# Performance work log

Measured on AMD Instinct MI355X. Metric: run time of the kernel, lower is better.

Reference implementation:

```python
import jax, jax.numpy as jnp
import numpy as np
from jax import lax

MAX_W = 4           # max_subword_block_width
DOWNSAMPLE = 2      # downsample_rate


def setup_inputs() -> dict:
    key = jax.random.key(0)
    k1, k2, k3, k4 = jax.random.split(key, 4)
    B, E, L, K = 8, 512, 4096, 5
    x = jax.random.normal(k1, (B, E, L), dtype=jnp.float32)
    conv_w = jax.random.normal(k2, (E, E, K), dtype=jnp.float32) * (1.0 / np.sqrt(E * K))
    conv_b = jax.random.normal(k3, (E,), dtype=jnp.float32) * 0.02
    score_w = jax.random.normal(k4, (E,), dtype=jnp.float32) * (1.0 / np.sqrt(E))
    return {"x": x, "conv_w": conv_w, "conv_b": conv_b, "score_w": score_w}


def reference(x, conv_w, conv_b, score_w):
    B, E, L = x.shape  # `length` captured BEFORE conv, as in the torch code
    # pre-GBST conv, VALID padding: length becomes L - K + 1
    y = lax.conv_general_dilated(
        x, conv_w, window_strides=(1,), padding='VALID',
        dimension_numbers=('NCH', 'OIH', 'NCH')) + conv_b[None, :, None]
    L2 = y.shape[-1]
    seqs, scores = [], []
    for w in range(1, MAX_W + 1):
        pad = (-L2) % w
        yp = jnp.pad(y, ((0, 0), (0, 0), (0, pad)))  # zero-pad to multiple of w
        nb = yp.shape[-1] // w
        pooled = yp.reshape(B, E, nb, w).mean(-1)          # avg_pool1d(kernel=w, stride=w)
        sc = jnp.einsum('ben,e->bn', pooled, score_w)      # Linear(E,1,bias=False)
        rs = jnp.repeat(pooled, w, axis=-1)                # repeat_interleave
        rsc = jnp.repeat(sc, w, axis=-1)
        cur = rs.shape[-1]
        if cur < L:  # re-pad with zeros up to the ORIGINAL (pre-conv) length
            rs = jnp.pad(rs, ((0, 0), (0, 0), (0, L - cur)))
            rsc = jnp.pad(rsc, ((0, 0), (0, L - cur)))
        seqs.append(rs[:, :, :L])
        scores.append(rsc[:, :L])
    S = jnp.stack(seqs, axis=-1)                           # [B,E,L,W]
    A = jax.nn.softmax(jnp.stack(scores, axis=-1), axis=-1)  # [B,L,W]
    out = jnp.einsum('belw,blw->bel', S, A)                # softmax-weighted combine
    r = DOWNSAMPLE
    Ld = (L // r) * r
    out = out[:, :, :Ld].reshape(B, E, L // r, r).mean(-1)  # final avg_pool1d
    return out
```

## Files before the change

### kernel.cpp

```cpp
#include <hip/hip_runtime.h>
#include <stdint.h>

#define E_DIM 512
#define L_IN  4096
#define L_OUT 4092
#define KW    5
#define B_DIM 8
#define L2P   4096
#define L_DS  2048
#define LP    4160

typedef __attribute__((ext_vector_type(8))) short short8;
typedef __attribute__((ext_vector_type(4))) float f32x4;

__device__ __forceinline__ unsigned short f2bf(float f) {
    uint32_t u = __float_as_uint(f);
    u += 0x7fffu + ((u >> 16) & 1);
    return (unsigned short)(u >> 16);
}
__device__ __forceinline__ float bf2f(unsigned short h) {
    return __uint_as_float((uint32_t)h << 16);
}

__global__ __launch_bounds__(256)
void xt_kernel(const float* __restrict__ x, unsigned short* __restrict__ Xt)
{
    const int b  = blockIdx.z;
    const int i0 = blockIdx.y * 64;
    const int l0 = blockIdx.x * 64;
    __shared__ float T[64][65];
    const int tid = threadIdx.x;

    const int ir = tid >> 4;
    const int cq = (tid & 15) * 4;
    #pragma unroll
    for (int jj = 0; jj < 4; ++jj) {
        int i = jj * 16 + ir;
        float4 v = make_float4(0.f, 0.f, 0.f, 0.f);
        if (l0 < L_IN)
            v = *reinterpret_cast<const float4*>(
                &x[((size_t)b * E_DIM + i0 + i) * L_IN + l0 + cq]);
        T[i][cq + 0] = v.x; T[i][cq + 1] = v.y;
        T[i][cq + 2] = v.z; T[i][cq + 3] = v.w;
    }
    __syncthreads();
    const int h  = tid & 31;
    const int rq = tid >> 5;
    #pragma unroll
    for (int j = 0; j < 8; ++j) {
        int lr = j * 8 + rq;
        ushort2 o;
        o.x = f2bf(T[2 * h][lr]);
        o.y = f2bf(T[2 * h + 1][lr]);
        *reinterpret_cast<ushort2*>(
            &Xt[((size_t)b * LP + l0 + lr) * E_DIM + i0 + 2 * h]) = o;
    }
}

__global__ __launch_bounds__(256)
void wt_kernel(const float* __restrict__ w, unsigned short* __restrict__ Wt)
{
    int idx = blockIdx.x * 256 + threadIdx.x;
    if (idx >= E_DIM * E_DIM) return;
    #pragma unroll
    for (int k = 0; k < KW; ++k)
        Wt[(size_t)k * E_DIM * E_DIM + idx] = f2bf(w[(size_t)idx * KW + k]);
}

#define XS_BYTES (144 * 64)
#define WS_OFF   XS_BYTES
#define WS_BYTES (5 * 128 * 64)
#define LDS_BYTES (XS_BYTES + WS_BYTES)
#define N_XCH (XS_BYTES / 1024)
#define N_CH  (LDS_BYTES / 1024)

__global__ __launch_bounds__(256, 3)
void conv_mfma(const unsigned short* __restrict__ Xt,
               const unsigned short* __restrict__ Wt,
               const float* __restrict__ bias,
               const float* __restrict__ sw,
               unsigned short* __restrict__ y,
               float* __restrict__ sp)
{
    __shared__ __align__(16) unsigned char lds[LDS_BYTES];
    const int l0 = blockIdx.x * 128;
    const int e0 = blockIdx.y * 128;
    const int b  = blockIdx.z;
    const int tid  = threadIdx.x;
    const int lane = tid & 63;
    const int wv   = tid >> 6;
    const int wr = wv >> 1, wc = wv & 1;
    const int lr = lane & 15, lg = lane >> 4;
    const int ln4r = lane >> 2;
    const int ln4c = (lane & 3) * 8;

    f32x4 acc[4][4] = {};

    for (int ks = 0; ks < 16; ++ks) {
        const int i0 = ks * 32;
        __syncthreads();
        for (int cch = wv; cch < N_CH; cch += 4) {
            void* lp = (void*)(lds + cch * 1024);
            const unsigned short* gp;
            if (cch < N_XCH) {
                int row = cch * 16 + ln4r;
                gp = Xt + ((size_t)b * LP + l0 + row) * E_DIM + i0 + ln4c;
            } else {
                int rk = (cch - N_XCH) * 16 + ln4r;
                int k = rk >> 7, er = rk & 127;
                gp = Wt + ((size_t)k * E_DIM + e0 + er) * E_DIM + i0 + ln4c;
            }
            __builtin_amdgcn_global_load_lds(
                (const __attribute__((address_space(1))) void*)gp,
                (__attribute__((address_space(3))) void*)lp,
                16, 0, 0);
        }
        __syncthreads();
        #pragma unroll
        for (int kt = 0; kt < KW; ++kt) {
            short8 aF[4], bF[4];
            #pragma unroll
            for (int m = 0; m < 4; ++m)
                aF[m] = *reinterpret_cast<const short8*>(
                    &lds[WS_OFF + (kt * 128 + wr * 64 + m * 16 + lr) * 64 + lg * 16]);
            #pragma unroll
            for (int n = 0; n < 4; ++n)
                bF[n] = *reinterpret_cast<const short8*>(
                    &lds[(wc * 64 + n * 16 + lr + kt) * 64 + lg * 16]);
            #pragma unroll
            for (int m = 0; m < 4; ++m)
                #pragma unroll
                for (int n = 0; n < 4; ++n)
                    acc[m][n] = __builtin_amdgcn_mfma_f32_16x16x32_bf16(
                        aF[m], bF[n], acc[m][n], 0, 0, 0);
        }
    }

    float spn[4] = {0.f, 0.f, 0.f, 0.f};
    #pragma unroll
    for (int m = 0; m < 4; ++m)
        #pragma unroll
        for (int q = 0; q < 4; ++q) {
            int e = e0 + wr * 64 + m * 16 + lg * 4 + q;
            float bv = bias[e];
            float wv_s = sw[e];
            unsigned short* yr =
                y + ((size_t)b * E_DIM + e) * L2P + l0 + wc * 64 + lr;
            #pragma unroll
            for (int n = 0; n < 4; ++n) {
                float v = acc[m][n][q] + bv;
                yr[n * 16] = f2bf(v);
                spn[n] = fmaf(v, wv_s, spn[n]);
            }
        }
    #pragma unroll
    for (int n = 0; n < 4; ++n) {
        float p = spn[n];
        p += __shfl_xor(p, 16);
        p += __shfl_xor(p, 32);
        if (lane < 16) {
            int l = l0 + wc * 64 + n * 16 + lane;
            sp[((size_t)b * L2P + l) * 8 + blockIdx.y * 2 + wr] = p;
        }
    }
}

__global__ __launch_bounds__(256)
void weight_kernel(const float* __restrict__ sp, float* __restrict__ A)
{
    const int b  = blockIdx.y;
    const int l0 = blockIdx.x * 256;
    const int tid = threadIdx.x;
    __shared__ float sl[260];

    for (int idx = tid; idx < 260; idx += 256) {
        int l = l0 - 2 + idx;
        float v = 0.f;
        if (l >= 0 && l < L_OUT) {
            const float* p = &sp[((size_t)b * L2P + l) * 8];
            v = ((p[0] + p[1]) + (p[2] + p[3])) + ((p[4] + p[5]) + (p[6] + p[7]));
        }
        sl[idx] = v;
    }
    __syncthreads();

    const int l = l0 + tid;
    if (l >= L_OUT) return;
    #define SL(i) sl[(i) - (l0 - 2)]
    float sc0 = SL(l);
    int n2 = l & ~1;
    float sc1 = 0.5f * (SL(n2) + SL(n2 + 1));
    int n3 = (l / 3) * 3;
    float sc2 = (1.f / 3.f) * (SL(n3) + SL(n3 + 1) + SL(n3 + 2));
    int n4 = l & ~3;
    float sc3 = 0.25f * (SL(n4) + SL(n4 + 1) + SL(n4 + 2) + SL(n4 + 3));
    #undef SL

    float m  = fmaxf(fmaxf(sc0, sc1), fmaxf(sc2, sc3));
    float e0 = __expf(sc0 - m), e1 = __expf(sc1 - m);
    float e2 = __expf(sc2 - m), e3 = __expf(sc3 - m);
    float inv = 1.f / (e0 + e1 + e2 + e3);

    float4 av = make_float4(e0 * inv, e1 * inv, e2 * inv, e3 * inv);
    *reinterpret_cast<float4*>(&A[((size_t)b * L2P + l) * 4]) = av;
}

typedef __attribute__((ext_vector_type(8))) unsigned short u16x8;

__global__ __launch_bounds__(256)
void combine_kernel(const unsigned short* __restrict__ y,
                    const float* __restrict__ A, float* __restrict__ out)
{
    const int e = blockIdx.x;
    const int b = blockIdx.y;
    const int tid = threadIdx.x;
    __shared__ float ys[L2P];

    const unsigned short* yrow = y + ((size_t)b * E_DIM + e) * L2P;
    #pragma unroll
    for (int j = 0; j < 2; ++j) {
        int base = (tid + j * 256) * 8;
        u16x8 v = *reinterpret_cast<const u16x8*>(&yrow[base]);
        #pragma unroll
        for (int t = 0; t < 8; ++t) ys[base + t] = bf2f(v[t]);
    }
    __syncthreads();

    const float* Ab = A + (size_t)b * L2P * 4;
    float* orow = out + ((size_t)b * E_DIM + e) * L_DS;
    #pragma unroll
    for (int j = 0; j < 8; ++j) {
        int m = tid + j * 256;
        float acc = 0.f;
        #pragma unroll
        for (int r = 0; r < 2; ++r) {
            int l = 2 * m + r;
            if (l < L_OUT) {
                const float4 a4 = *reinterpret_cast<const float4*>(&Ab[l * 4]);
                float t = a4.x * ys[l];
                int n2 = l & ~1;
                t += a4.y * 0.5f * (ys[n2] + ys[n2 + 1]);
                int n3 = (l / 3) * 3;
                t += a4.z * (1.f / 3.f) * (ys[n3] + ys[n3 + 1] + ys[n3 + 2]);
                int n4 = l & ~3;
                t += a4.w * 0.25f * (ys[n4] + ys[n4 + 1] + ys[n4 + 2] + ys[n4 + 3]);
                acc += t;
            }
        }
        orow[m] = 0.5f * acc;
    }
}

extern "C" void kernel_launch(void* const* d_in, const int* in_sizes, int n_in,
                              void* d_out, int out_size, void* d_ws, size_t ws_size,
                              hipStream_t stream)
{
    const float* x  = (const float*)d_in[0];
    const float* w  = (const float*)d_in[1];
    const float* bb = (const float*)d_in[2];
    const float* sw = (const float*)d_in[3];
    float* out = (float*)d_out;

    unsigned short* Y = (unsigned short*)d_ws;
    float* SP = (float*)(Y + (size_t)B_DIM * E_DIM * L2P);
    float* A  = SP + (size_t)B_DIM * L2P * 8;
    unsigned short* Xt = (unsigned short*)(A + (size_t)B_DIM * L2P * 4);
    unsigned short* Wt = Xt + (size_t)B_DIM * LP * E_DIM;

    xt_kernel<<<dim3(LP / 64, E_DIM / 64, B_DIM), 256, 0, stream>>>(x, Xt);
    wt_kernel<<<dim3(E_DIM * E_DIM / 256), 256, 0, stream>>>(w, Wt);
    conv_mfma<<<dim3(L2P / 128, E_DIM / 128, B_DIM), 256, 0, stream>>>(Xt, Wt, bb, sw, Y, SP);
    weight_kernel<<<dim3(L2P / 256, B_DIM), 256, 0, stream>>>(SP, A);
    combine_kernel<<<dim3(E_DIM, B_DIM), 256, 0, stream>>>(Y, A, out);
}
```

Measured before the change: 140.1 us.

## Software-pipeline conv MFMA loads with double-buffered X and rotating weight slots

```diff
diff --git a/kernel.cpp b/kernel.cpp
--- a/kernel.cpp
+++ b/kernel.cpp
@@ -21,6 +21,11 @@
 __device__ __forceinline__ float bf2f(unsigned short h) {
     return __uint_as_float((uint32_t)h << 16);
 }
+__device__ __forceinline__ int mod3(int v) {
+    if (v >= 6) v -= 6;
+    if (v >= 3) v -= 3;
+    return v;
+}
 
 __global__ __launch_bounds__(256)
 void xt_kernel(const float* __restrict__ x, unsigned short* __restrict__ Xt)
@@ -67,12 +72,11 @@
         Wt[(size_t)k * E_DIM * E_DIM + idx] = f2bf(w[(size_t)idx * KW + k]);
 }
 
-#define XS_BYTES (144 * 64)
-#define WS_OFF   XS_BYTES
-#define WS_BYTES (5 * 128 * 64)
-#define LDS_BYTES (XS_BYTES + WS_BYTES)
-#define N_XCH (XS_BYTES / 1024)
-#define N_CH  (LDS_BYTES / 1024)
+#define XB_ROWS  144
+#define XB_BYTES (XB_ROWS * 64)
+#define WOFF     (2 * XB_BYTES)
+#define WSL      8192
+#define LDS_BYTES (WOFF + 3 * WSL)
 
 __global__ __launch_bounds__(256, 3)
 void conv_mfma(const unsigned short* __restrict__ Xt,
@@ -92,48 +96,104 @@
     const int wr = wv >> 1, wc = wv & 1;
     const int lr = lane & 15, lg = lane >> 4;
     const int ln4r = lane >> 2;
-    const int ln4c = (lane & 3) * 8;
-
-    f32x4 acc[4][4] = {};
-
-    for (int ks = 0; ks < 16; ++ks) {
-        const int i0 = ks * 32;
-        __syncthreads();
-        for (int cch = wv; cch < N_CH; cch += 4) {
-            void* lp = (void*)(lds + cch * 1024);
-            const unsigned short* gp;
-            if (cch < N_XCH) {
-                int row = cch * 16 + ln4r;
-                gp = Xt + ((size_t)b * LP + l0 + row) * E_DIM + i0 + ln4c;
-            } else {
-                int rk = (cch - N_XCH) * 16 + ln4r;
-                int k = rk >> 7, er = rk & 127;
-                gp = Wt + ((size_t)k * E_DIM + e0 + er) * E_DIM + i0 + ln4c;
-            }
+    const int xswz = ((lane & 3) ^ ((lane >> 3) & 3)) * 8;
+    const int swz  = (lg ^ ((lr >> 1) & 3)) << 4;
+
+    const unsigned short* xt_base =
+        Xt + ((size_t)b * LP + l0) * E_DIM + xswz;
+
+    auto stageW = [&](int slot, int tap, int i0) {
+        for (int c = wv; c < 8; c += 4) {
+            int er = c * 16 + ln4r;
+            const unsigned short* gp =
+                Wt + ((size_t)tap * E_DIM + e0 + er) * E_DIM + i0 + xswz;
             __builtin_amdgcn_global_load_lds(
                 (const __attribute__((address_space(1))) void*)gp,
-                (__attribute__((address_space(3))) void*)lp,
+                (__attribute__((address_space(3))) void*)(lds + WOFF + slot * WSL + c * 1024),
                 16, 0, 0);
         }
-        __syncthreads();
+    };
+    auto stageX1 = [&](int buf, int i0, int cch) {
+        int row = cch * 16 + ln4r;
+        const unsigned short* gp = xt_base + (size_t)row * E_DIM + i0;
+        __builtin_amdgcn_global_load_lds(
+            (const __attribute__((address_space(1))) void*)gp,
+            (__attribute__((address_space(3))) void*)(lds + buf * XB_BYTES + cch * 1024),
+            16, 0, 0);
+    };
+
+    f32x4 acc[4][4] = {};
+
+    stageX1(0, 0, wv); stageX1(0, 0, wv + 4);
+    if (wv == 0) stageX1(0, 0, 8);
+    stageW(0, 0, 0);
+    stageW(1, 1, 0);
+    asm volatile("s_waitcnt vmcnt(0)" ::: "memory");
+    __builtin_amdgcn_s_barrier();
+
+    int s0 = 0;
+    for (int ks = 0; ks < 16; ++ks) {
+        const int par  = ks & 1;
+        const int xoff = par * XB_BYTES;
+        const int i0n  = (ks + 1) * 32;
+        const bool more = (ks < 15);
         #pragma unroll
         for (int kt = 0; kt < KW; ++kt) {
+            const int slot = mod3(s0 + kt);
             short8 aF[4], bF[4];
             #pragma unroll
             for (int m = 0; m < 4; ++m)
                 aF[m] = *reinterpret_cast<const short8*>(
-                    &lds[WS_OFF + (kt * 128 + wr * 64 + m * 16 + lr) * 64 + lg * 16]);
+                    &lds[WOFF + slot * WSL + (wr * 64 + m * 16 + lr) * 64 + swz]);
             #pragma unroll
-            for (int n = 0; n < 4; ++n)
+            for (int n = 0; n < 4; ++n) {
+                const int rB = wc * 64 + n * 16 + lr + kt;
                 bF[n] = *reinterpret_cast<const short8*>(
-                    &lds[(wc * 64 + n * 16 + lr + kt) * 64 + lg * 16]);
+                    &lds[xoff + rB * 64 + ((lg ^ ((rB >> 1) & 3)) << 4)]);
+            }
+
+            if (kt == 0) {
+                stageW(mod3(s0 + 2), 2, ks * 32);
+                if (more) stageX1(par ^ 1, i0n, wv);
+            } else if (kt == 1) {
+                stageW(mod3(s0 + 3), 3, ks * 32);
+                if (more) { stageX1(par ^ 1, i0n, wv + 4);
+                            if (wv == 0) stageX1(par ^ 1, i0n, 8); }
+            } else if (kt == 2) {
+                stageW(mod3(s0 + 4), 4, ks * 32);
+            } else if (kt == 3) {
+                if (more) stageW(mod3(s0 + 5), 0, i0n);
+            } else {
+                if (more) stageW(mod3(s0 + 6), 1, i0n);
+            }
+
+            if (kt == 0) {
+                if (more) asm volatile("s_waitcnt vmcnt(3)" ::: "memory");
+                else      asm volatile("s_waitcnt vmcnt(2)" ::: "memory");
+            } else if (kt == 1) {
+                if (more) {
+                    if (wv == 0) asm volatile("s_waitcnt vmcnt(4)" ::: "memory");
+                    else         asm volatile("s_waitcnt vmcnt(3)" ::: "memory");
+                } else           asm volatile("s_waitcnt vmcnt(2)" ::: "memory");
+            } else if (kt == 2) {
+                asm volatile("s_waitcnt vmcnt(2)" ::: "memory");
+            } else {
+                if (more) asm volatile("s_waitcnt vmcnt(2)" ::: "memory");
+                else      asm volatile("s_waitcnt vmcnt(0)" ::: "memory");
+            }
+            __builtin_amdgcn_s_barrier();
+
+            __builtin_amdgcn_s_setprio(1);
             #pragma unroll
             for (int m = 0; m < 4; ++m)
                 #pragma unroll
                 for (int n = 0; n < 4; ++n)
                     acc[m][n] = __builtin_amdgcn_mfma_f32_16x16x32_bf16(
                         aF[m], bF[n], acc[m][n], 0, 0, 0);
-        }
+            __builtin_amdgcn_s_setprio(0);
+            __builtin_amdgcn_s_barrier();
+        }
+        s0 += 2; if (s0 >= 3) s0 -= 3;
     }
 
     float spn[4] = {0.f, 0.f, 0.f, 0.f};
```

New measurement: 126.0 us. 1.11x faster.
